# Kernel tuning notes

Hardware: AMD Instinct MI355X
Metric: run time of the kernel (lower is better)

## Reference

```python
import jax, jax.numpy as jnp
import numpy as np

N_NODES = 20000


def setup_inputs() -> dict:
    key = jax.random.key(0)
    ks = jax.random.split(key, 6)
    d = 512
    E = 640000
    x = jax.random.normal(ks[0], (N_NODES, d), dtype=jnp.float32)
    edge_index = jax.random.randint(ks[1], (2, E), 0, N_NODES, dtype=jnp.int64)
    s = 1.0 / np.sqrt(d)
    W1 = jax.random.uniform(ks[2], (d, d), jnp.float32, -s, s)
    b1 = jax.random.uniform(ks[3], (d,), jnp.float32, -s, s)
    W2 = jax.random.uniform(ks[4], (d, d), jnp.float32, -s, s)
    b2 = jax.random.uniform(ks[5], (d,), jnp.float32, -s, s)
    return {"x": x, "edge_index": edge_index, "W1": W1, "b1": b1, "W2": W2, "b2": b2}


def reference(x, edge_index, W1, b1, W2, b2):
    eps = 0.0
    src, dst = edge_index[0], edge_index[1]
    # scatter-add neighbor aggregation: sum_{j in N(i)} x_j
    agg = jax.ops.segment_sum(x[src], dst, num_segments=N_NODES)  # [N, d]
    h = (1.0 + eps) * x + agg
    # MLP: Linear -> ReLU -> Linear
    h = jax.nn.relu(h @ W1 + b1)
    out = h @ W2 + b2
    return out
```

## Files before the change

kernel.cpp:

```cpp
#include <hip/hip_runtime.h>
#include <hip/hip_bf16.h>

typedef __attribute__((ext_vector_type(8))) short s16x8;
typedef __attribute__((ext_vector_type(4))) float f32x4;
typedef __attribute__((ext_vector_type(2))) float pf2;

#define D_FEAT 512
#define SLICES 8
#define SLICE_D 64
#define ROWS 80

__device__ __forceinline__ unsigned short f2bf(float f) {
  __hip_bfloat16 h = __float2bfloat16(f);
  return *reinterpret_cast<unsigned short*>(&h);
}

__device__ __forceinline__ float bitsf(unsigned int u) {
  union { unsigned int i; float f; } c;
  c.i = u;
  return c.f;
}

__device__ __forceinline__ void async16(void* lds, const void* g) {
  __builtin_amdgcn_global_load_lds(
      (const __attribute__((address_space(1))) void*)g,
      (__attribute__((address_space(3))) void*)lds, 16, 0, 0);
}


__global__ __launch_bounds__(256) void zero_k(int4* __restrict__ p, int n16) {
  int i = blockIdx.x * 256 + threadIdx.x;
  if (i < n16) p[i] = make_int4(0, 0, 0, 0);
}


__global__ __launch_bounds__(256) void hx_k(const int* __restrict__ dst, int E,
                                            int* __restrict__ deg) {
  int i4 = (blockIdx.x * 256 + threadIdx.x) * 4;
  if (i4 + 3 < E) {
    int4 d4 = *(const int4*)&dst[i4];
    atomicAdd(&deg[d4.x], 1);
    atomicAdd(&deg[d4.y], 1);
    atomicAdd(&deg[d4.z], 1);
    atomicAdd(&deg[d4.w], 1);
  } else {
    for (int i = i4; i < E; ++i) atomicAdd(&deg[dst[i]], 1);
  }
}


__global__ __launch_bounds__(1024) void scanw_k(const int* __restrict__ deg,
                                                int* __restrict__ rowstart,
                                                unsigned short* __restrict__ nodeord, int n,
                                                const float* __restrict__ W1,
                                                const float* __restrict__ W2,
                                                unsigned short* __restrict__ W1t,
                                                unsigned short* __restrict__ W2t,
                                                const float* __restrict__ x,
                                                unsigned short* __restrict__ xs, int n8) {
  if (blockIdx.x < 128) {
    __shared__ float tile[64][65];
    int t = blockIdx.x;
    const float* W = W1;
    unsigned short* Wt = W1t;
    if (t >= 64) { t -= 64; W = W2; Wt = W2t; }
    int tr = (t >> 3) * 64;
    int tc = (t & 7) * 64;
    int tid = threadIdx.x;
    int c4 = (tid & 15) * 4, r = tid >> 4;
    float4 vv = *(const float4*)&W[(size_t)(tr + r) * 512 + tc + c4];
    tile[r][c4] = vv.x; tile[r][c4 + 1] = vv.y; tile[r][c4 + 2] = vv.z; tile[r][c4 + 3] = vv.w;
    __syncthreads();
    int nn = tid >> 4;
    int k0 = (tid & 15) * 4;
    ushort4 o;
    o.x = f2bf(tile[k0 + 0][nn]);
    o.y = f2bf(tile[k0 + 1][nn]);
    o.z = f2bf(tile[k0 + 2][nn]);
    o.w = f2bf(tile[k0 + 3][nn]);
    *(ushort4*)&Wt[(size_t)(tc + nn) * 512 + tr + k0] = o;
    return;
  }
  if (blockIdx.x > 128) {
    int i = (blockIdx.x - 129) * 1024 + threadIdx.x;
    if (i < n8) {
      int nd = i >> 6;
      int c = i & 63;
      int s = c >> 3;
      int off = c & 7;
      const float4* p = (const float4*)x + (size_t)i * 2;
      float4 u = p[0], v = p[1];
      s16x8 r;
      r[0] = (short)f2bf(u.x); r[1] = (short)f2bf(u.y);
      r[2] = (short)f2bf(u.z); r[3] = (short)f2bf(u.w);
      r[4] = (short)f2bf(v.x); r[5] = (short)f2bf(v.y);
      r[6] = (short)f2bf(v.z); r[7] = (short)f2bf(v.w);
      ((s16x8*)xs)[((size_t)s * n + nd) * 8 + off] = r;
    }
    return;
  }
  __shared__ int wsum[16];
  __shared__ int carry_s;
  __shared__ int hist[65];
  int tid = threadIdx.x;
  int lane = tid & 63, wid = tid >> 6;
  if (tid == 0) carry_s = 0;
  __syncthreads();
  for (int t0 = 0; t0 < n; t0 += 4096) {
    int base = t0 + tid * 4;
    int e0, e1, e2, e3;
    if (base + 3 < n) {
      int4 v4 = *(const int4*)&deg[base];
      e0 = v4.x; e1 = v4.y; e2 = v4.z; e3 = v4.w;
    } else {
      e0 = (base + 0 < n) ? deg[base + 0] : 0;
      e1 = (base + 1 < n) ? deg[base + 1] : 0;
      e2 = (base + 2 < n) ? deg[base + 2] : 0;
      e3 = (base + 3 < n) ? deg[base + 3] : 0;
    }
    int lsum = e0 + e1 + e2 + e3;
    int s = lsum;
#pragma unroll
    for (int off = 1; off < 64; off <<= 1) {
      int t = __shfl_up(s, off);
      if (lane >= off) s += t;
    }
    if (lane == 63) wsum[wid] = s;
    __syncthreads();
    if (wid == 0) {
      int ws = (lane < 16) ? wsum[lane] : 0;
#pragma unroll
      for (int off = 1; off < 16; off <<= 1) {
        int t = __shfl_up(ws, off);
        if (lane >= off) ws += t;
      }
      if (lane < 16) wsum[lane] = ws;
    }
    __syncthreads();
    int carry = carry_s;
    int wbase = (wid > 0) ? wsum[wid - 1] : 0;
    int pre = carry + wbase + (s - lsum);
    if (base + 0 < n) rowstart[base + 0] = pre;
    if (base + 1 < n) rowstart[base + 1] = pre + e0;
    if (base + 2 < n) rowstart[base + 2] = pre + e0 + e1;
    if (base + 3 < n) rowstart[base + 3] = pre + e0 + e1 + e2;
    int total = wsum[15];
    __syncthreads();
    if (tid == 0) carry_s = carry + total;
    __syncthreads();
  }
  if (tid == 0) rowstart[n] = carry_s;
  if (tid < 65) hist[tid] = 0;
  __syncthreads();
  for (int i = tid; i < n; i += 1024) atomicAdd(&hist[min(deg[i], 64)], 1);
  __syncthreads();
  if (tid == 0) {
    int run = 0;
    for (int b = 0; b < 65; ++b) { int c = hist[b]; hist[b] = run; run += c; }
  }
  __syncthreads();
  for (int i = tid; i < n; i += 1024) {
    int b = min(deg[i], 64);
    int pos = atomicAdd(&hist[b], 1);
    nodeord[pos] = (unsigned short)i;
  }
}


__global__ __launch_bounds__(256) void fill_k(const int* __restrict__ src,
                                              const int* __restrict__ dst, int E,
                                              const int* __restrict__ rowstart,
                                              int* __restrict__ cursor,
                                              unsigned short* __restrict__ ep16) {
  int i4 = (blockIdx.x * 256 + threadIdx.x) * 4;
  if (i4 + 3 < E) {
    int4 d4 = *(const int4*)&dst[i4];
    int4 s4 = *(const int4*)&src[i4];
    int p0 = atomicAdd(&cursor[d4.x], 1); ep16[rowstart[d4.x] + p0] = (unsigned short)s4.x;
    int p1 = atomicAdd(&cursor[d4.y], 1); ep16[rowstart[d4.y] + p1] = (unsigned short)s4.y;
    int p2 = atomicAdd(&cursor[d4.z], 1); ep16[rowstart[d4.z] + p2] = (unsigned short)s4.z;
    int p3 = atomicAdd(&cursor[d4.w], 1); ep16[rowstart[d4.w] + p3] = (unsigned short)s4.w;
  } else {
    for (int i = i4; i < E; ++i) {
      int d = dst[i];
      int pos = atomicAdd(&cursor[d], 1);
      ep16[rowstart[d] + pos] = (unsigned short)src[i];
    }
  }
}


__global__ __launch_bounds__(256, 8) void agg_k(const unsigned short* __restrict__ xs,
                                                const int* __restrict__ rowstart,
                                                const unsigned short* __restrict__ ep16,
                                                const unsigned short* __restrict__ nodeord,
                                                unsigned short* __restrict__ h, int Nn) {
  int slice = blockIdx.x & 7;
  int nb = blockIdx.x >> 3;
  int wid = threadIdx.x >> 6, lane = threadIdx.x & 63;
  int g = lane >> 3, sub = lane & 7;
  int slot = (nb * 4 + wid) * 8 + g;
  int node = nodeord[slot];
  int beg = rowstart[node];
  int deg = rowstart[node + 1] - beg;
  int degm1 = max(deg - 1, 0);
  int dm = deg;
  dm = max(dm, __shfl_xor(dm, 8));
  dm = max(dm, __shfl_xor(dm, 16));
  dm = max(dm, __shfl_xor(dm, 32));
  const unsigned short* ep = ep16 + beg;
  const s16x8* sb = (const s16x8*)xs + (size_t)slice * Nn * 8;
  s16x8 own = sb[node * 8 + sub];
  pf2 acc[4];
#pragma unroll
  for (int q = 0; q < 4; ++q) {
    unsigned int d = (unsigned int)((const int*)&own)[q];
    acc[q].x = bitsf(d << 16);
    acc[q].y = bitsf(d & 0xffff0000u);
  }
  for (int t = 0; t < dm; t += 4) {
    s16x8 v[4];
    float m[4];
#pragma unroll
    for (int b = 0; b < 4; ++b) {
      int tt = t + b;
      int e = ep[min(tt, degm1)];
      m[b] = (tt < deg) ? 1.f : 0.f;
      v[b] = sb[e * 8 + sub];
    }
#pragma unroll
    for (int b = 0; b < 4; ++b) {
#pragma unroll
      for (int q = 0; q < 4; ++q) {
        unsigned int d = (unsigned int)((const int*)&v[b])[q];
        pf2 p;
        p.x = bitsf(d << 16);
        p.y = bitsf(d & 0xffff0000u);
        acc[q] += m[b] * p;
      }
    }
  }
  s16x8 r;
#pragma unroll
  for (int q = 0; q < 4; ++q) {
    r[q * 2 + 0] = (short)f2bf(acc[q].x);
    r[q * 2 + 1] = (short)f2bf(acc[q].y);
  }
  __builtin_nontemporal_store(r, (s16x8*)(h + (size_t)node * D_FEAT + slice * SLICE_D + sub * 8));
}


__global__ __launch_bounds__(1024, 1) void mlp_k(const unsigned short* __restrict__ A,
                                                 const unsigned short* __restrict__ W1t,
                                                 const unsigned short* __restrict__ W2t,
                                                 const float* __restrict__ b1,
                                                 const float* __restrict__ b2,
                                                 float* __restrict__ out, int M) {
  __shared__ unsigned short As[2][ROWS * 32];
  __shared__ unsigned short Bs[2][512 * 32];
  __shared__ unsigned short c1s[ROWS * 512];
  int tm = blockIdx.x;
  int tid = threadIdx.x;
  int wave = tid >> 6, lane = tid & 63;
  int lr = lane & 15, lh = lane >> 4;
  bool aw = tid < 320;

  auto ldschunk = [](int row, int c) {
    int p = row >> 1;
    return p * 8 + (((((row & 1) << 2) | c)) ^ (p & 7));
  };

  auto stage_b = [&](const unsigned short* Bt, int pb, int k0) {
#pragma unroll
    for (int ii = 0; ii < 2; ++ii) {
      int cb = ii * 1024 + tid;
      int p = cb >> 3;
      int s2 = (cb & 7) ^ (p & 7);
      int row = p * 2 + (s2 >> 2);
      int c = s2 & 3;
      async16(&Bs[pb][(size_t)(ii * 1024 + wave * 64) * 8], Bt + (size_t)row * 512 + k0 + c * 8);
    }
  };
  auto stage_a = [&](int pb, int k0) {
    if (aw) {
      int cb = tid;
      int p = cb >> 3;
      int s2 = (cb & 7) ^ (p & 7);
      int row = p * 2 + (s2 >> 2);
      int c = s2 & 3;
      int ga = min(tm * ROWS + row, M - 1);
      async16(&As[pb][(size_t)(wave * 64) * 8], A + (size_t)ga * 512 + k0 + c * 8);
    }
  };

  f32x4 zero = {0.f, 0.f, 0.f, 0.f};
  f32x4 acc[5][2];
#pragma unroll
  for (int rt = 0; rt < 5; ++rt)
#pragma unroll
    for (int ct = 0; ct < 2; ++ct) acc[rt][ct] = zero;

  stage_b(W1t, 0, 0);
  stage_a(0, 0);
#pragma unroll
  for (int t = 0; t < 16; ++t) {
    int pb = t & 1;
    if (t < 15) { stage_b(W1t, pb ^ 1, (t + 1) * 32); stage_a(pb ^ 1, (t + 1) * 32); }
    if (t < 15) {
      if (aw) asm volatile("s_waitcnt vmcnt(3)" ::: "memory");
      else    asm volatile("s_waitcnt vmcnt(2)" ::: "memory");
    } else {
      asm volatile("s_waitcnt vmcnt(0)" ::: "memory");
    }
    __builtin_amdgcn_s_barrier();
    s16x8 av[5], bv[2];
#pragma unroll
    for (int rt = 0; rt < 5; ++rt)
      av[rt] = *(const s16x8*)&As[pb][ldschunk(rt * 16 + lr, lh) * 8];
#pragma unroll
    for (int ct = 0; ct < 2; ++ct)
      bv[ct] = *(const s16x8*)&Bs[pb][ldschunk(wave * 32 + ct * 16 + lr, lh) * 8];
#pragma unroll
    for (int rt = 0; rt < 5; ++rt)
#pragma unroll
      for (int ct = 0; ct < 2; ++ct)
        acc[rt][ct] = __builtin_amdgcn_mfma_f32_16x16x32_bf16(av[rt], bv[ct], acc[rt][ct], 0, 0, 0);
    __builtin_amdgcn_s_barrier();
  }

  stage_b(W2t, 0, 0);

#pragma unroll
  for (int ct = 0; ct < 2; ++ct) {
    int col = wave * 32 + ct * 16 + lr;
    float bval = b1[col];
    int chunk = col >> 3;
#pragma unroll
    for (int rt = 0; rt < 5; ++rt) {
#pragma unroll
      for (int j = 0; j < 4; ++j) {
        int row = rt * 16 + lh * 4 + j;
        float v = fmaxf(acc[rt][ct][j] + bval, 0.f);
        c1s[row * 512 + ((chunk ^ (row & 7)) * 8) + (col & 7)] = f2bf(v);
      }
    }
  }
  __syncthreads();

#pragma unroll
  for (int rt = 0; rt < 5; ++rt)
#pragma unroll
    for (int ct = 0; ct < 2; ++ct) acc[rt][ct] = zero;

#pragma unroll
  for (int t = 0; t < 16; ++t) {
    int pb = t & 1;
    if (t < 15) stage_b(W2t, pb ^ 1, (t + 1) * 32);
    if (t < 15) asm volatile("s_waitcnt vmcnt(2)" ::: "memory");
    else        asm volatile("s_waitcnt vmcnt(0)" ::: "memory");
    __builtin_amdgcn_s_barrier();
    s16x8 av[5], bv[2];
#pragma unroll
    for (int rt = 0; rt < 5; ++rt) {
      int row = rt * 16 + lr;
      av[rt] = *(const s16x8*)&c1s[row * 512 + (((t * 4 + lh) ^ (row & 7)) * 8)];
    }
#pragma unroll
    for (int ct = 0; ct < 2; ++ct)
      bv[ct] = *(const s16x8*)&Bs[pb][ldschunk(wave * 32 + ct * 16 + lr, lh) * 8];
#pragma unroll
    for (int rt = 0; rt < 5; ++rt)
#pragma unroll
      for (int ct = 0; ct < 2; ++ct)
        acc[rt][ct] = __builtin_amdgcn_mfma_f32_16x16x32_bf16(av[rt], bv[ct], acc[rt][ct], 0, 0, 0);
    __builtin_amdgcn_s_barrier();
  }

#pragma unroll
  for (int ct = 0; ct < 2; ++ct) {
    int col = wave * 32 + ct * 16 + lr;
    float bval = b2[col];
#pragma unroll
    for (int rt = 0; rt < 5; ++rt) {
#pragma unroll
      for (int j = 0; j < 4; ++j) {
        int row = tm * ROWS + rt * 16 + lh * 4 + j;
        if (row < M)
          __builtin_nontemporal_store(acc[rt][ct][j] + bval, &out[(size_t)row * 512 + col]);
      }
    }
  }
}


extern "C" void kernel_launch(void* const* d_in, const int* in_sizes, int n_in,
                              void* d_out, int out_size, void* d_ws, size_t ws_size,
                              hipStream_t stream) {
  const float* x = (const float*)d_in[0];
  const int* ei = (const int*)d_in[1];
  const float* W1 = (const float*)d_in[2];
  const float* b1 = (const float*)d_in[3];
  const float* W2 = (const float*)d_in[4];
  const float* b2 = (const float*)d_in[5];
  const int N = in_sizes[0] / D_FEAT;
  const int E = in_sizes[1] / 2;
  const int* src = ei;
  const int* dst = ei + E;

  char* w = (char*)d_ws;
  auto alloc = [&](size_t bytes) {
    void* p = (void*)w;
    w += (bytes + 255) & ~(size_t)255;
    return p;
  };
  unsigned short* ep16 = (unsigned short*)alloc((size_t)E * 2 + 256);
  int* deg = (int*)alloc((size_t)N * 4);
  int* cursor = (int*)alloc((size_t)N * 4);
  int* rowstart = (int*)alloc((size_t)(N + 1) * 4);
  unsigned short* nodeord = (unsigned short*)alloc((size_t)N * 2);
  unsigned short* W1t = (unsigned short*)alloc((size_t)512 * 512 * 2);
  unsigned short* W2t = (unsigned short*)alloc((size_t)512 * 512 * 2);
  unsigned short* h = (unsigned short*)alloc((size_t)N * 512 * 2);
  unsigned short* xs = (unsigned short*)d_out + (size_t)N * D_FEAT;

  size_t zbytes = (size_t)((char*)cursor - (char*)deg) + (size_t)N * 4;
  int zn16 = (int)(zbytes / 16);
  zero_k<<<(zn16 + 255) / 256, 256, 0, stream>>>((int4*)deg, zn16);
  int hb4 = (E / 4 + 255) / 256;
  hx_k<<<hb4, 256, 0, stream>>>(dst, E, deg);
  int n8 = N * D_FEAT / 8;
  int xbk = (n8 + 1023) / 1024;
  scanw_k<<<129 + xbk, 1024, 0, stream>>>(deg, rowstart, nodeord, N, W1, W2, W1t, W2t,
                                          x, xs, n8);
  fill_k<<<hb4, 256, 0, stream>>>(src, dst, E, rowstart, cursor, ep16);
  agg_k<<<8 * (N / 32), 256, 0, stream>>>(xs, rowstart, ep16, nodeord, h, N);
  int mt = (N + ROWS - 1) / ROWS;
  mlp_k<<<mt, 1024, 0, stream>>>(h, W1t, W2t, b1, b2, (float*)d_out, N);
}
```

Baseline: 173.0 us.

## Fuse degree histogram with weight/x conversion; split scan into single-pass kernel

Result: faster. 168.5 us, median of 2 (-2.6%).

```diff
diff --git a/kernel.cpp b/kernel.cpp
--- a/kernel.cpp
+++ b/kernel.cpp
@@ -9,6 +9,7 @@
 #define SLICES 8
 #define SLICE_D 64
 #define ROWS 80
+#define NPT 20
 
 __device__ __forceinline__ unsigned short f2bf(float f) {
   __hip_bfloat16 h = __float2bfloat16(f);
@@ -34,129 +35,146 @@
 }
 
 
-__global__ __launch_bounds__(256) void hx_k(const int* __restrict__ dst, int E,
-                                            int* __restrict__ deg) {
-  int i4 = (blockIdx.x * 256 + threadIdx.x) * 4;
-  if (i4 + 3 < E) {
-    int4 d4 = *(const int4*)&dst[i4];
-    atomicAdd(&deg[d4.x], 1);
-    atomicAdd(&deg[d4.y], 1);
-    atomicAdd(&deg[d4.z], 1);
-    atomicAdd(&deg[d4.w], 1);
-  } else {
-    for (int i = i4; i < E; ++i) atomicAdd(&deg[dst[i]], 1);
-  }
-}
-
-
-__global__ __launch_bounds__(1024) void scanw_k(const int* __restrict__ deg,
-                                                int* __restrict__ rowstart,
-                                                unsigned short* __restrict__ nodeord, int n,
-                                                const float* __restrict__ W1,
-                                                const float* __restrict__ W2,
-                                                unsigned short* __restrict__ W1t,
-                                                unsigned short* __restrict__ W2t,
-                                                const float* __restrict__ x,
-                                                unsigned short* __restrict__ xs, int n8) {
-  if (blockIdx.x < 128) {
+__global__ __launch_bounds__(256) void prep_k(const int* __restrict__ dst, int E,
+                                              int* __restrict__ deg,
+                                              const float* __restrict__ W1,
+                                              const float* __restrict__ W2,
+                                              unsigned short* __restrict__ W1t,
+                                              unsigned short* __restrict__ W2t,
+                                              const float* __restrict__ x,
+                                              unsigned short* __restrict__ xs,
+                                              int n8, int Nn) {
+  int bid = blockIdx.x;
+  if (bid < 625) {
+    int i4 = (bid * 256 + threadIdx.x) * 4;
+    if (i4 + 3 < E) {
+      int4 d4 = *(const int4*)&dst[i4];
+      atomicAdd(&deg[d4.x], 1);
+      atomicAdd(&deg[d4.y], 1);
+      atomicAdd(&deg[d4.z], 1);
+      atomicAdd(&deg[d4.w], 1);
+    } else {
+      for (int i = i4; i < E; ++i) atomicAdd(&deg[dst[i]], 1);
+    }
+    return;
+  }
+  if (bid < 753) {
     __shared__ float tile[64][65];
-    int t = blockIdx.x;
+    int t = bid - 625;
     const float* W = W1;
     unsigned short* Wt = W1t;
     if (t >= 64) { t -= 64; W = W2; Wt = W2t; }
     int tr = (t >> 3) * 64;
     int tc = (t & 7) * 64;
     int tid = threadIdx.x;
-    int c4 = (tid & 15) * 4, r = tid >> 4;
-    float4 vv = *(const float4*)&W[(size_t)(tr + r) * 512 + tc + c4];
-    tile[r][c4] = vv.x; tile[r][c4 + 1] = vv.y; tile[r][c4 + 2] = vv.z; tile[r][c4 + 3] = vv.w;
+    int c4 = (tid & 15) * 4, rg = tid >> 4;
+#pragma unroll
+    for (int rr = 0; rr < 64; rr += 16) {
+      int r = rr + rg;
+      float4 vv = *(const float4*)&W[(size_t)(tr + r) * 512 + tc + c4];
+      tile[r][c4] = vv.x; tile[r][c4 + 1] = vv.y; tile[r][c4 + 2] = vv.z; tile[r][c4 + 3] = vv.w;
+    }
     __syncthreads();
-    int nn = tid >> 4;
-    int k0 = (tid & 15) * 4;
-    ushort4 o;
-    o.x = f2bf(tile[k0 + 0][nn]);
-    o.y = f2bf(tile[k0 + 1][nn]);
-    o.z = f2bf(tile[k0 + 2][nn]);
-    o.w = f2bf(tile[k0 + 3][nn]);
-    *(ushort4*)&Wt[(size_t)(tc + nn) * 512 + tr + k0] = o;
+    int ch = tid & 15;
+#pragma unroll
+    for (int rr = 0; rr < 64; rr += 16) {
+      int nn = rr + rg;
+      int k0 = ch * 4;
+      ushort4 o;
+      o.x = f2bf(tile[k0 + 0][nn]);
+      o.y = f2bf(tile[k0 + 1][nn]);
+      o.z = f2bf(tile[k0 + 2][nn]);
+      o.w = f2bf(tile[k0 + 3][nn]);
+      *(ushort4*)&Wt[(size_t)(tc + nn) * 512 + tr + k0] = o;
+    }
     return;
   }
-  if (blockIdx.x > 128) {
-    int i = (blockIdx.x - 129) * 1024 + threadIdx.x;
-    if (i < n8) {
-      int nd = i >> 6;
-      int c = i & 63;
-      int s = c >> 3;
-      int off = c & 7;
-      const float4* p = (const float4*)x + (size_t)i * 2;
-      float4 u = p[0], v = p[1];
-      s16x8 r;
-      r[0] = (short)f2bf(u.x); r[1] = (short)f2bf(u.y);
-      r[2] = (short)f2bf(u.z); r[3] = (short)f2bf(u.w);
-      r[4] = (short)f2bf(v.x); r[5] = (short)f2bf(v.y);
-      r[6] = (short)f2bf(v.z); r[7] = (short)f2bf(v.w);
-      ((s16x8*)xs)[((size_t)s * n + nd) * 8 + off] = r;
-    }
-    return;
-  }
+  int i = (bid - 753) * 256 + threadIdx.x;
+  if (i < n8) {
+    int nd = i >> 6;
+    int c = i & 63;
+    int s = c >> 3;
+    int off = c & 7;
+    const float4* p = (const float4*)x + (size_t)i * 2;
+    float4 u = p[0], v = p[1];
+    s16x8 r;
+    r[0] = (short)f2bf(u.x); r[1] = (short)f2bf(u.y);
+    r[2] = (short)f2bf(u.z); r[3] = (short)f2bf(u.w);
+    r[4] = (short)f2bf(v.x); r[5] = (short)f2bf(v.y);
+    r[6] = (short)f2bf(v.z); r[7] = (short)f2bf(v.w);
+    ((s16x8*)xs)[((size_t)s * Nn + nd) * 8 + off] = r;
+  }
+}
+
+
+__global__ __launch_bounds__(1024) void scan_k(const int* __restrict__ deg,
+                                               int* __restrict__ rowstart,
+                                               unsigned short* __restrict__ nodeord, int n) {
   __shared__ int wsum[16];
-  __shared__ int carry_s;
   __shared__ int hist[65];
   int tid = threadIdx.x;
   int lane = tid & 63, wid = tid >> 6;
-  if (tid == 0) carry_s = 0;
-  __syncthreads();
-  for (int t0 = 0; t0 < n; t0 += 4096) {
-    int base = t0 + tid * 4;
-    int e0, e1, e2, e3;
-    if (base + 3 < n) {
-      int4 v4 = *(const int4*)&deg[base];
-      e0 = v4.x; e1 = v4.y; e2 = v4.z; e3 = v4.w;
+  int base = tid * NPT;
+  int e[NPT];
+#pragma unroll
+  for (int q = 0; q < NPT / 4; ++q) {
+    int b4 = base + q * 4;
+    if (b4 + 3 < n) {
+      int4 v4 = *(const int4*)&deg[b4];
+      e[q * 4 + 0] = v4.x; e[q * 4 + 1] = v4.y; e[q * 4 + 2] = v4.z; e[q * 4 + 3] = v4.w;
     } else {
-      e0 = (base + 0 < n) ? deg[base + 0] : 0;
-      e1 = (base + 1 < n) ? deg[base + 1] : 0;
-      e2 = (base + 2 < n) ? deg[base + 2] : 0;
-      e3 = (base + 3 < n) ? deg[base + 3] : 0;
-    }
-    int lsum = e0 + e1 + e2 + e3;
-    int s = lsum;
-#pragma unroll
-    for (int off = 1; off < 64; off <<= 1) {
-      int t = __shfl_up(s, off);
-      if (lane >= off) s += t;
-    }
-    if (lane == 63) wsum[wid] = s;
-    __syncthreads();
-    if (wid == 0) {
-      int ws = (lane < 16) ? wsum[lane] : 0;
-#pragma unroll
-      for (int off = 1; off < 16; off <<= 1) {
-        int t = __shfl_up(ws, off);
-        if (lane >= off) ws += t;
-      }
-      if (lane < 16) wsum[lane] = ws;
-    }
-    __syncthreads();
-    int carry = carry_s;
-    int wbase = (wid > 0) ? wsum[wid - 1] : 0;
-    int pre = carry + wbase + (s - lsum);
-    if (base + 0 < n) rowstart[base + 0] = pre;
-    if (base + 1 < n) rowstart[base + 1] = pre + e0;
-    if (base + 2 < n) rowstart[base + 2] = pre + e0 + e1;
-    if (base + 3 < n) rowstart[base + 3] = pre + e0 + e1 + e2;
-    int total = wsum[15];
-    __syncthreads();
-    if (tid == 0) carry_s = carry + total;
-    __syncthreads();
-  }
-  if (tid == 0) rowstart[n] = carry_s;
+      e[q * 4 + 0] = (b4 + 0 < n) ? deg[b4 + 0] : 0;
+      e[q * 4 + 1] = (b4 + 1 < n) ? deg[b4 + 1] : 0;
+      e[q * 4 + 2] = (b4 + 2 < n) ? deg[b4 + 2] : 0;
+      e[q * 4 + 3] = (b4 + 3 < n) ? deg[b4 + 3] : 0;
+    }
+  }
+  int lsum = 0;
+#pragma unroll
+  for (int q = 0; q < NPT; ++q) lsum += e[q];
+  int s = lsum;
+#pragma unroll
+  for (int off = 1; off < 64; off <<= 1) {
+    int t = __shfl_up(s, off);
+    if (lane >= off) s += t;
+  }
+  if (lane == 63) wsum[wid] = s;
+  __syncthreads();
+  if (wid == 0) {
+    int ws = (lane < 16) ? wsum[lane] : 0;
+#pragma unroll
+    for (int off = 1; off < 16; off <<= 1) {
+      int t = __shfl_up(ws, off);
+      if (lane >= off) ws += t;
+    }
+    if (lane < 16) wsum[lane] = ws;
+  }
+  __syncthreads();
+  int pre = ((wid > 0) ? wsum[wid - 1] : 0) + (s - lsum);
+  int run = pre;
+  int pfx[NPT];
+#pragma unroll
+  for (int q = 0; q < NPT; ++q) { pfx[q] = run; run += e[q]; }
+#pragma unroll
+  for (int q = 0; q < NPT / 4; ++q) {
+    int b4 = base + q * 4;
+    if (b4 + 3 < n) {
+      *(int4*)&rowstart[b4] = make_int4(pfx[q * 4 + 0], pfx[q * 4 + 1], pfx[q * 4 + 2], pfx[q * 4 + 3]);
+    } else {
+      if (b4 + 0 < n) rowstart[b4 + 0] = pfx[q * 4 + 0];
+      if (b4 + 1 < n) rowstart[b4 + 1] = pfx[q * 4 + 1];
+      if (b4 + 2 < n) rowstart[b4 + 2] = pfx[q * 4 + 2];
+      if (b4 + 3 < n) rowstart[b4 + 3] = pfx[q * 4 + 3];
+    }
+  }
+  if (tid == 1023) rowstart[n] = run;
   if (tid < 65) hist[tid] = 0;
   __syncthreads();
   for (int i = tid; i < n; i += 1024) atomicAdd(&hist[min(deg[i], 64)], 1);
   __syncthreads();
   if (tid == 0) {
-    int run = 0;
-    for (int b = 0; b < 65; ++b) { int c = hist[b]; hist[b] = run; run += c; }
+    int r2 = 0;
+    for (int b = 0; b < 65; ++b) { int c = hist[b]; hist[b] = r2; r2 += c; }
   }
   __syncthreads();
   for (int i = tid; i < n; i += 1024) {
@@ -426,12 +444,11 @@
   size_t zbytes = (size_t)((char*)cursor - (char*)deg) + (size_t)N * 4;
   int zn16 = (int)(zbytes / 16);
   zero_k<<<(zn16 + 255) / 256, 256, 0, stream>>>((int4*)deg, zn16);
+  int n8 = N * D_FEAT / 8;
+  int xbk = (n8 + 255) / 256;
+  prep_k<<<753 + xbk, 256, 0, stream>>>(dst, E, deg, W1, W2, W1t, W2t, x, xs, n8, N);
+  scan_k<<<1, 1024, 0, stream>>>(deg, rowstart, nodeord, N);
   int hb4 = (E / 4 + 255) / 256;
-  hx_k<<<hb4, 256, 0, stream>>>(dst, E, deg);
-  int n8 = N * D_FEAT / 8;
-  int xbk = (n8 + 1023) / 1024;
-  scanw_k<<<129 + xbk, 1024, 0, stream>>>(deg, rowstart, nodeord, N, W1, W2, W1t, W2t,
-                                          x, xs, n8);
   fill_k<<<hb4, 256, 0, stream>>>(src, dst, E, rowstart, cursor, ep16);
   agg_k<<<8 * (N / 32), 256, 0, stream>>>(xs, rowstart, ep16, nodeord, h, N);
   int mt = (N + ROWS - 1) / ROWS;
```
